# Kernel optimization log

Measured on AMD Instinct MI355X. Metric: run time of the kernel, lower is better.

The kernel has to match this reference:

```python
import jax, jax.numpy as jnp
import numpy as np

B, N, F_IN, F_OUT, E = 8, 20000, 128, 128, 320000
ALPHA = 0.2  # LeakyReLU negative slope


def _xavier_normal(key, shape, gain=1.414):
    fan_in, fan_out = shape[0], shape[1]
    std = gain * np.sqrt(2.0 / (fan_in + fan_out))
    return jax.random.normal(key, shape, dtype=jnp.float32) * std


def setup_inputs() -> dict:
    key = jax.random.key(0)
    k1, k2, k3, k4, k5 = jax.random.split(key, 5)
    x = jax.random.normal(k1, (B, N, F_IN), dtype=jnp.float32)
    W = _xavier_normal(k2, (F_IN, F_OUT))
    a = _xavier_normal(k3, (2 * F_OUT, 1))
    # Edge list (src, dst). First N src are arange so every row has >=1 edge
    # (avoids div-by-zero in rowsum, matching a graph with no isolated sources).
    src_extra = jax.random.randint(k4, (E - N,), 0, N, dtype=jnp.int32)
    src = jnp.concatenate([jnp.arange(N, dtype=jnp.int32), src_extra])
    dst = jax.random.randint(k5, (E,), 0, N, dtype=jnp.int32)
    edge = jnp.stack([src, dst], axis=0)  # [2, E]
    return {"x": x, "W": W, "a": a, "edge": edge}


def reference(x, W, a, edge):
    # x: [B, N, F_in], W: [F_in, F_out], a: [2*F_out, 1], edge: [2, E]
    Fo = W.shape[1]
    n = x.shape[1]
    src, dst = edge[0], edge[1]
    h = jnp.einsum('bnf,fo->bno', x, W)  # [B, N, Fo]
    # cat(h[src], h[dst]) @ a  ==  (h @ a1)[src] + (h @ a2)[dst]
    a1, a2 = a[:Fo, 0], a[Fo:, 0]
    s = (h @ a1)[:, src] + (h @ a2)[:, dst]  # [B, E]
    score = jnp.where(s > 0, s, ALPHA * s)  # LeakyReLU
    e = jnp.exp(-score)  # [B, E]
    # spmm: h_prime[src] += e * h[dst]; rowsum[src] += e  (per batch)
    msg = e[..., None] * h[:, dst, :]  # [B, E, Fo]
    seg = jax.vmap(lambda m: jax.ops.segment_sum(m, src, num_segments=n))(msg)  # [B,N,Fo]
    rowsum = jax.vmap(lambda v: jax.ops.segment_sum(v, src, num_segments=n))(e)  # [B,N]
    h_prime = seg / rowsum[..., None]
    return jax.nn.elu(h_prime)  # concat=True -> ELU
```

## Files before the change

### kernel.cpp

```cpp
#include <hip/hip_runtime.h>

#define NB 8
#define NN 20000
#define FI 128
#define FO 128
#define NE 320000
#define ROWS (NB * NN)
#define LRALPHA 0.2f
#define ELLW 96

typedef short bf16x8 __attribute__((ext_vector_type(8)));
typedef float f32x4 __attribute__((ext_vector_type(4)));

static __device__ __forceinline__ float b2f(unsigned short u) {
  return __uint_as_float(((unsigned int)u) << 16);
}
static __device__ __forceinline__ unsigned short f2b(float f) {
  unsigned int u = __float_as_uint(f);
  return (unsigned short)((u + 0x7FFFu + ((u >> 16) & 1u)) >> 16);
}

__global__ __launch_bounds__(256) void wt_kernel(const float* __restrict__ W,
                                                 unsigned short* __restrict__ Wb,
                                                 int* __restrict__ cursor) {
  int idx = blockIdx.x * 256 + threadIdx.x;
  if (idx < FI * FO) {
    int k = idx >> 7, o = idx & 127;
    Wb[o * 128 + k] = f2b(W[idx]);
  }
  if (idx < NN) cursor[idx] = 0;
}

#define LDW 136

__global__ __launch_bounds__(256) void gemm_kernel(
    const float* __restrict__ x, const unsigned short* __restrict__ Wb,
    const float* __restrict__ a,
    unsigned short* __restrict__ hb,
    float* __restrict__ g1, float* __restrict__ g2) {
  __shared__ __align__(16) unsigned short Ws[128 * LDW];
  const int tid = threadIdx.x;

  {
    const bf16x8* wsrc = (const bf16x8*)Wb;
#pragma unroll
    for (int it = 0; it < 8; ++it) {
      int c = tid + it * 256;
      int o = c >> 4, seg = c & 15;
      *(bf16x8*)&Ws[o * LDW + seg * 8] = wsrc[c];
    }
  }

  const int wv = tid >> 6;
  const int lane = tid & 63;
  const int m = lane & 15;
  const int quad = lane >> 4;
  const size_t row0 = (size_t)blockIdx.x * 64 + wv * 16;

  const float* xr = x + (row0 + m) * 128;
  bf16x8 afr[4];
#pragma unroll
  for (int k0 = 0; k0 < 4; ++k0) {
    const float4* xp = (const float4*)(xr + k0 * 32 + quad * 8);
    float4 v0 = xp[0];
    float4 v1 = xp[1];
    union { bf16x8 v; unsigned short u[8]; } af;
    af.u[0] = f2b(v0.x); af.u[1] = f2b(v0.y);
    af.u[2] = f2b(v0.z); af.u[3] = f2b(v0.w);
    af.u[4] = f2b(v1.x); af.u[5] = f2b(v1.y);
    af.u[6] = f2b(v1.z); af.u[7] = f2b(v1.w);
    afr[k0] = af.v;
  }
  __syncthreads();

  f32x4 acc[8] = {};
#pragma unroll
  for (int k0 = 0; k0 < 4; ++k0) {
#pragma unroll
    for (int c = 0; c < 8; ++c) {
      bf16x8 bf = *(const bf16x8*)&Ws[(c * 16 + m) * LDW + k0 * 32 + quad * 8];
      acc[c] = __builtin_amdgcn_mfma_f32_16x16x32_bf16(afr[k0], bf, acc[c], 0, 0, 0);
    }
  }

  unsigned short* hp = hb + row0 * 128;
#pragma unroll
  for (int c = 0; c < 8; ++c)
#pragma unroll
    for (int r = 0; r < 4; ++r)
      hp[(quad * 4 + r) * 128 + c * 16 + m] = f2b(acc[c][r]);

  float a1v[8], a2v[8];
#pragma unroll
  for (int c = 0; c < 8; ++c) {
    a1v[c] = a[c * 16 + m];
    a2v[c] = a[128 + c * 16 + m];
  }
  float p1[4] = {}, p2[4] = {};
#pragma unroll
  for (int c = 0; c < 8; ++c)
#pragma unroll
    for (int r = 0; r < 4; ++r) {
      p1[r] = fmaf(acc[c][r], a1v[c], p1[r]);
      p2[r] = fmaf(acc[c][r], a2v[c], p2[r]);
    }
#pragma unroll
  for (int off = 1; off < 16; off <<= 1)
#pragma unroll
    for (int r = 0; r < 4; ++r) {
      p1[r] += __shfl_xor(p1[r], off, 64);
      p2[r] += __shfl_xor(p2[r], off, 64);
    }
  if (m == 0) {
    size_t rbase = row0 + quad * 4;
#pragma unroll
    for (int r = 0; r < 4; ++r) {
      g1[rbase + r] = p1[r];
      g2[rbase + r] = p2[r];
    }
  }
}

__global__ __launch_bounds__(256) void ell_scatter_kernel(
    const int* __restrict__ src, const int* __restrict__ dst,
    int* __restrict__ cursor, int* __restrict__ ell) {
  int e = blockIdx.x * 256 + threadIdx.x;
  if (e < NE) {
    int s = src[e];
    int d = dst[e];
    int slot = atomicAdd(&cursor[s], 1);
    if (slot < ELLW) ell[s * ELLW + slot] = d;
  }
}

__global__ __launch_bounds__(256) void gather_kernel(
    const unsigned short* __restrict__ hb, const float* __restrict__ g1,
    const float* __restrict__ g2, const int* __restrict__ degs,
    const int* __restrict__ ell, float* __restrict__ out) {
  const int bid = blockIdx.x;
  const int b = bid & 7;
  const int wv = threadIdx.x >> 6;
  const int i = (bid >> 3) * 4 + wv;
  const int lane = threadIdx.x & 63;
  const int group = lane >> 3;
  const int sub = lane & 7;
  const int deg = min(degs[i], ELLW);
  const int base = i * ELLW;
  const float g1i = g1[(size_t)b * NN + i];
  const float* g2b = g2 + (size_t)b * NN;
  const unsigned short* hbb = hb + (size_t)b * NN * 128;

  float acc[16] = {};
  float rs = 0.f;
  for (int c0 = 0; c0 < deg; c0 += 64) {
    const int cnt = min(64, deg - c0);
    const int li = lane < cnt ? lane : cnt - 1;
    const int dvec = ell[base + c0 + li];
    float w = 0.f;
    if (lane < cnt) {
      float sv = g1i + g2b[dvec];
      float sc = fmaxf(sv, LRALPHA * sv);
      w = __expf(-sc);
    }
    rs += w;
    const int iters = (cnt + 7) >> 3;
    for (int t = 0; t < iters; ++t) {
      const int sel = t * 8 + group;
      float wg = __shfl(w, sel, 64);
      int dg = __shfl(dvec, sel, 64);
      const bf16x8* hp = (const bf16x8*)(hbb + (size_t)dg * 128 + sub * 16);
      union { bf16x8 v; unsigned short u[8]; } h0, h1;
      h0.v = hp[0];
      h1.v = hp[1];
#pragma unroll
      for (int k = 0; k < 8; ++k) {
        acc[k]     = fmaf(wg, b2f(h0.u[k]), acc[k]);
        acc[8 + k] = fmaf(wg, b2f(h1.u[k]), acc[8 + k]);
      }
    }
  }
#pragma unroll
  for (int k = 0; k < 16; ++k) {
    acc[k] += __shfl_xor(acc[k], 8, 64);
    acc[k] += __shfl_xor(acc[k], 16, 64);
    acc[k] += __shfl_xor(acc[k], 32, 64);
  }
#pragma unroll
  for (int off = 1; off < 64; off <<= 1) rs += __shfl_xor(rs, off, 64);

  if (lane < 8) {
    float inv = 1.f / rs;
    float o[16];
#pragma unroll
    for (int k = 0; k < 16; ++k) {
      float v = acc[k] * inv;
      o[k] = v > 0.f ? v : expm1f(v);
    }
    float4* op = (float4*)(out + ((size_t)b * NN + i) * 128 + sub * 16);
    op[0] = make_float4(o[0], o[1], o[2], o[3]);
    op[1] = make_float4(o[4], o[5], o[6], o[7]);
    op[2] = make_float4(o[8], o[9], o[10], o[11]);
    op[3] = make_float4(o[12], o[13], o[14], o[15]);
  }
}

extern "C" void kernel_launch(void* const* d_in, const int* in_sizes, int n_in,
                              void* d_out, int out_size, void* d_ws, size_t ws_size,
                              hipStream_t stream) {
  const float* x = (const float*)d_in[0];
  const float* W = (const float*)d_in[1];
  const float* a = (const float*)d_in[2];
  const int* edge = (const int*)d_in[3];
  const int* src = edge;
  const int* dst = edge + NE;
  float* out = (float*)d_out;

  char* p = (char*)d_ws;
  unsigned short* hb = (unsigned short*)p;  p += (size_t)ROWS * 128 * 2;
  float* g1 = (float*)p;                    p += (size_t)ROWS * 4;
  float* g2 = (float*)p;                    p += (size_t)ROWS * 4;
  int* cursor = (int*)p;                    p += (size_t)NN * 4;
  int* ell = (int*)p;                       p += (size_t)NN * ELLW * 4;
  unsigned short* Wb = (unsigned short*)p;  p += (size_t)FI * FO * 2;

  wt_kernel<<<80, 256, 0, stream>>>(W, Wb, cursor);
  gemm_kernel<<<ROWS / 64, 256, 0, stream>>>(x, Wb, a, hb, g1, g2);
  ell_scatter_kernel<<<(NE + 255) / 256, 256, 0, stream>>>(src, dst, cursor, ell);
  gather_kernel<<<(NN / 4) * NB, 256, 0, stream>>>(hb, g1, g2, cursor, ell, out);
}
```

Measured before the change: 289.8 us.

## Remap gather so each lane owns two features across all edges

The gather kernel now has each of the 64 lanes accumulate two bf16 features over every neighbor edge in turn. The old layout split edges across 8 lane groups of 16 features each. This drops the cross-group shuffle reduction and lets all 64 lanes do the ELU and a coalesced float2 store. The cost is eight times more loop iterations, each with two shuffles and a narrow 4-byte load. The ELU also switches from expm1f to __expf(v)-1, a small precision change.

Result: faster. 260.1 us (-10.3%).

```diff
diff --git a/kernel.cpp b/kernel.cpp
--- a/kernel.cpp
+++ b/kernel.cpp
@@ -142,15 +142,13 @@
   const int wv = threadIdx.x >> 6;
   const int i = (bid >> 3) * 4 + wv;
   const int lane = threadIdx.x & 63;
-  const int group = lane >> 3;
-  const int sub = lane & 7;
   const int deg = min(degs[i], ELLW);
   const int base = i * ELLW;
   const float g1i = g1[(size_t)b * NN + i];
   const float* g2b = g2 + (size_t)b * NN;
-  const unsigned short* hbb = hb + (size_t)b * NN * 128;
-
-  float acc[16] = {};
+  const char* hrow = (const char*)(hb + (size_t)b * NN * 128) + lane * 4;
+
+  float accLo = 0.f, accHi = 0.f;
   float rs = 0.f;
   for (int c0 = 0; c0 < deg; c0 += 64) {
     const int cnt = min(64, deg - c0);
@@ -163,45 +161,28 @@
       w = __expf(-sc);
     }
     rs += w;
-    const int iters = (cnt + 7) >> 3;
-    for (int t = 0; t < iters; ++t) {
-      const int sel = t * 8 + group;
-      float wg = __shfl(w, sel, 64);
-      int dg = __shfl(dvec, sel, 64);
-      const bf16x8* hp = (const bf16x8*)(hbb + (size_t)dg * 128 + sub * 16);
-      union { bf16x8 v; unsigned short u[8]; } h0, h1;
-      h0.v = hp[0];
-      h1.v = hp[1];
-#pragma unroll
-      for (int k = 0; k < 8; ++k) {
-        acc[k]     = fmaf(wg, b2f(h0.u[k]), acc[k]);
-        acc[8 + k] = fmaf(wg, b2f(h1.u[k]), acc[8 + k]);
+    const int cr = (cnt + 3) & ~3;
+    for (int j = 0; j < cr; j += 4) {
+#pragma unroll
+      for (int jj = 0; jj < 4; ++jj) {
+        float wj = __shfl(w, j + jj, 64);
+        int dj = __shfl(dvec, j + jj, 64);
+        unsigned int u = *(const unsigned int*)(hrow + ((size_t)dj << 8));
+        accLo = fmaf(wj, __uint_as_float(u << 16), accLo);
+        accHi = fmaf(wj, __uint_as_float(u & 0xFFFF0000u), accHi);
       }
     }
   }
 #pragma unroll
-  for (int k = 0; k < 16; ++k) {
-    acc[k] += __shfl_xor(acc[k], 8, 64);
-    acc[k] += __shfl_xor(acc[k], 16, 64);
-    acc[k] += __shfl_xor(acc[k], 32, 64);
-  }
-#pragma unroll
   for (int off = 1; off < 64; off <<= 1) rs += __shfl_xor(rs, off, 64);
 
-  if (lane < 8) {
-    float inv = 1.f / rs;
-    float o[16];
-#pragma unroll
-    for (int k = 0; k < 16; ++k) {
-      float v = acc[k] * inv;
-      o[k] = v > 0.f ? v : expm1f(v);
-    }
-    float4* op = (float4*)(out + ((size_t)b * NN + i) * 128 + sub * 16);
-    op[0] = make_float4(o[0], o[1], o[2], o[3]);
-    op[1] = make_float4(o[4], o[5], o[6], o[7]);
-    op[2] = make_float4(o[8], o[9], o[10], o[11]);
-    op[3] = make_float4(o[12], o[13], o[14], o[15]);
-  }
+  const float inv = 1.f / rs;
+  float v0 = accLo * inv;
+  float v1 = accHi * inv;
+  float o0 = v0 > 0.f ? v0 : __expf(v0) - 1.f;
+  float o1 = v1 > 0.f ? v1 : __expf(v1) - 1.f;
+  float2* op = (float2*)(out + ((size_t)b * NN + i) * 128 + lane * 2);
+  *op = make_float2(o0, o1);
 }
 
 extern "C" void kernel_launch(void* const* d_in, const int* in_sizes, int n_in,
```
